# Kernel optimization log

Measured on AMD Instinct MI355X. Metric: run time of the kernel, lower is better.

## Reference

```python
import jax, jax.numpy as jnp
import numpy as np

NUM_HEADS = 12


def setup_inputs() -> dict:
    key = jax.random.key(0)
    ks = jax.random.split(key, 5)
    B, N, C = 64, 388, 768  # N = 8*8*2 + 16*16 + 4
    return {
        "x": jax.random.normal(ks[0], (B, N, C), dtype=jnp.float32),
        "qkv_w": jax.random.normal(ks[1], (3 * C, C), dtype=jnp.float32) * 0.02,
        "qkv_b": jax.random.normal(ks[2], (3 * C,), dtype=jnp.float32) * 0.02,
        "proj_w": jax.random.normal(ks[3], (C, C), dtype=jnp.float32) * 0.02,
        "proj_b": jax.random.normal(ks[4], (C,), dtype=jnp.float32) * 0.02,
        "t_h": 8, "t_w": 8, "s_h": 16, "s_w": 16,
    }


def reference(x, qkv_w, qkv_b, proj_w, proj_b, t_h, t_w, s_h, s_w):
    B, N, C = x.shape
    H = NUM_HEADS
    D = C // H
    scale = D ** -0.5
    L_t = t_h * t_w * 2          # template (x2) tokens
    L_s = s_h * s_w + 4          # search tokens + 4 extra

    qkv = x @ qkv_w.T + qkv_b                       # [B,N,3C]
    qkv = qkv.reshape(B, N, 3, H, D).transpose(2, 0, 3, 1, 4)  # [3,B,H,N,D]
    q, k, v = qkv[0], qkv[1], qkv[2]                # each [B,H,N,D]

    q_mt, q_s = q[:, :, :L_t], q[:, :, L_t:]
    k_mt = k[:, :, :L_t]
    v_mt = v[:, :, :L_t]

    # template self-attention (template queries attend only to template keys)
    attn_mt = jax.nn.softmax(jnp.einsum("bhqd,bhkd->bhqk", q_mt, k_mt) * scale, axis=-1)
    x_mt = jnp.einsum("bhqk,bhkd->bhqd", attn_mt, v_mt)  # [B,H,L_t,D]
    x_mt = x_mt.transpose(0, 2, 1, 3).reshape(B, L_t, C)

    # search queries attend to ALL keys
    attn_s = jax.nn.softmax(jnp.einsum("bhqd,bhkd->bhqk", q_s, k) * scale, axis=-1)
    x_s = jnp.einsum("bhqk,bhkd->bhqd", attn_s, v)  # [B,H,L_s,D]
    x_s = x_s.transpose(0, 2, 1, 3).reshape(B, L_s, C)

    out = jnp.concatenate([x_mt, x_s], axis=1)      # [B,N,C]
    out = out @ proj_w.T + proj_b
    return out
```

## Files before the change

kernel.cpp:

```cpp
#include <hip/hip_runtime.h>
#include <cstdint>
#include <cstddef>
#include <cmath>

typedef __attribute__((ext_vector_type(4))) float f32x4;
typedef __attribute__((ext_vector_type(8))) short bf16x8;

typedef const __attribute__((address_space(1))) void* gas_ptr;
typedef __attribute__((address_space(3))) void* las_ptr;

static __device__ __forceinline__ short f2bf(float f) {
    __bf16 h = (__bf16)f;
    return __builtin_bit_cast(short, h);
}

constexpr int MP = 25088;

__global__ void cvt_all(const float* __restrict__ x,  const float* __restrict__ qw,
                        const float* __restrict__ pw,
                        short* __restrict__ xb, short* __restrict__ qwb,
                        short* __restrict__ pwb)
{
    constexpr int NX = MP * 768 / 4;
    constexpr int NQ = 2304 * 768 / 4;
    constexpr int NP = 768 * 768 / 4;
    constexpr int NT = NX + NQ + NP;
    int i = blockIdx.x * blockDim.x + threadIdx.x;
    const int stride = gridDim.x * blockDim.x;
    for (; i < NT; i += stride) {
        if (i < NX) {
            const int flat = i * 4;
            const int mp  = flat / 768;
            const int col = flat - mp * 768;
            const int b   = mp / 392;
            const int nn  = mp - b * 392;
            short4 o;
            if (nn < 388) {
                const float4 v = *reinterpret_cast<const float4*>(
                    x + ((size_t)(b * 388 + nn) * 768 + col));
                o.x = f2bf(v.x); o.y = f2bf(v.y); o.z = f2bf(v.z); o.w = f2bf(v.w);
            } else {
                o.x = 0; o.y = 0; o.z = 0; o.w = 0;
            }
            reinterpret_cast<short4*>(xb)[i] = o;
        } else if (i < NX + NQ) {
            const int j = i - NX;
            const float4 v = reinterpret_cast<const float4*>(qw)[j];
            short4 o;
            o.x = f2bf(v.x); o.y = f2bf(v.y); o.z = f2bf(v.z); o.w = f2bf(v.w);
            reinterpret_cast<short4*>(qwb)[j] = o;
        } else {
            const int j = i - NX - NQ;
            const float4 v = reinterpret_cast<const float4*>(pw)[j];
            short4 o;
            o.x = f2bf(v.x); o.y = f2bf(v.y); o.z = f2bf(v.z); o.w = f2bf(v.w);
            reinterpret_cast<short4*>(pwb)[j] = o;
        }
    }
}

__global__ __launch_bounds__(512, 2) void gemm_qkv256(
    const short* __restrict__ A, const short* __restrict__ Bw,
    const float* __restrict__ bias,
    short* __restrict__ qk, short* __restrict__ vT)
{
    constexpr int K = 768;
    constexpr int KT = 12;
    __shared__ __align__(16) short lds[2][2][256 * 64];

    const int tid  = threadIdx.x;
    const int lane = tid & 63;
    const int wid  = tid >> 6;
    const int lrow = lane & 15;
    const int lgrp = lane >> 4;
    const int wr   = wid >> 2;
    const int wc   = wid & 3;

    const int nwg = gridDim.x;
    const int q8  = nwg >> 3, r8 = nwg & 7;
    const int xcd = blockIdx.x & 7, bidx = blockIdx.x >> 3;
    const int wgid = (xcd < r8 ? xcd * (q8 + 1) : r8 * (q8 + 1) + (xcd - r8) * q8) + bidx;
    constexpr int G = 14, SG = G * 9;
    const int mg  = wgid / SG;
    const int r_  = wgid - mg * SG;
    const int nn_ = r_ / G;
    const int mi  = r_ - nn_ * G;
    const int m0  = (mg * G + mi) * 256;
    const int n0  = nn_ * 256;

    f32x4 acc[8][4];
    #pragma unroll
    for (int i = 0; i < 8; ++i)
        #pragma unroll
        for (int j = 0; j < 4; ++j)
            acc[i][j] = f32x4{0.f, 0.f, 0.f, 0.f};

    auto stage = [&](int kt, int buf) {
        #pragma unroll
        for (int it = 0; it < 4; ++it) {
            const int c   = it * 512 + tid;
            const int row = c >> 3;
            const int scb = ((c & 7) * 16) ^ ((row & 7) << 4);
            const short* ga = A  + (size_t)(m0 + row) * K + kt * 64 + (scb >> 1);
            const short* gb = Bw + (size_t)(n0 + row) * K + kt * 64 + (scb >> 1);
            __builtin_amdgcn_global_load_lds((gas_ptr)ga, (las_ptr)((char*)&lds[buf][0][0] + c * 16), 16, 0, 0);
            __builtin_amdgcn_global_load_lds((gas_ptr)gb, (las_ptr)((char*)&lds[buf][1][0] + c * 16), 16, 0, 0);
        }
    };

    stage(0, 0);

    for (int kt = 0; kt < KT; ++kt) {
        const int cur = kt & 1;
        if (kt + 1 < KT) {
            stage(kt + 1, cur ^ 1);
            asm volatile("s_waitcnt vmcnt(8)" ::: "memory");
        } else {
            asm volatile("s_waitcnt vmcnt(0)" ::: "memory");
        }
        __builtin_amdgcn_s_barrier();
        __builtin_amdgcn_sched_barrier(0);

        #pragma unroll
        for (int ks = 0; ks < 2; ++ks) {
            bf16x8 af[8], bfv[4];
            #pragma unroll
            for (int i = 0; i < 8; ++i) {
                const int r   = wr * 128 + i * 16 + lrow;
                const int byt = r * 128 + ((ks * 64 + lgrp * 16) ^ ((r & 7) << 4));
                af[i] = *reinterpret_cast<const bf16x8*>((const char*)&lds[cur][0][0] + byt);
            }
            #pragma unroll
            for (int j = 0; j < 4; ++j) {
                const int r   = wc * 64 + j * 16 + lrow;
                const int byt = r * 128 + ((ks * 64 + lgrp * 16) ^ ((r & 7) << 4));
                bfv[j] = *reinterpret_cast<const bf16x8*>((const char*)&lds[cur][1][0] + byt);
            }
            #pragma unroll
            for (int i = 0; i < 8; ++i)
                #pragma unroll
                for (int j = 0; j < 4; ++j)
                    acc[i][j] = __builtin_amdgcn_mfma_f32_16x16x32_bf16(af[i], bfv[j], acc[i][j], 0, 0, 0);
        }

        __builtin_amdgcn_sched_barrier(0);
        __builtin_amdgcn_s_barrier();
    }

    const int mb = m0 + wr * 128;
    const int nb = n0 + wc * 64;
    if (n0 < 1536) {
        #pragma unroll
        for (int j = 0; j < 4; ++j) {
            const int c  = nb + j * 16 + lrow;
            const float sc = (c < 768) ? 0.18033688011116f : 1.0f;
            const float bv = bias[c];
            #pragma unroll
            for (int i = 0; i < 8; ++i) {
                #pragma unroll
                for (int r = 0; r < 4; ++r) {
                    const int m = mb + i * 16 + lgrp * 4 + r;
                    qk[(size_t)m * 1536 + c] = f2bf((acc[i][j][r] + bv) * sc);
                }
            }
        }
    } else {
        const int h = (nb - 1536) >> 6;
        short* lw = (short*)&lds[0][0][0] + wid * (64 * 80);
        #pragma unroll
        for (int pass = 0; pass < 2; ++pass) {
            if (pass) {
                asm volatile("s_waitcnt lgkmcnt(0)" ::: "memory");
                __builtin_amdgcn_sched_barrier(0);
            }
            #pragma unroll
            for (int j = 0; j < 4; ++j) {
                const int dloc = j * 16 + lrow;
                const float bv = bias[nb + j * 16 + lrow];
                #pragma unroll
                for (int ii = 0; ii < 4; ++ii)
                    #pragma unroll
                    for (int r = 0; r < 4; ++r)
                        lw[dloc * 80 + ii * 16 + lgrp * 4 + r] = f2bf(acc[pass * 4 + ii][j][r] + bv);
            }
            asm volatile("s_waitcnt lgkmcnt(0)" ::: "memory");
            __builtin_amdgcn_sched_barrier(0);
            #pragma unroll
            for (int w = 0; w < 8; ++w) {
                const int d    = w * 8 + (lane >> 3);
                const int nloc = (lane & 7) * 8;
                const bf16x8 val = *reinterpret_cast<const bf16x8*>(lw + d * 80 + nloc);
                const int mchunk = mb + pass * 64 + nloc;
                const int b  = mchunk / 392;
                const int nn = mchunk - b * 392;
                short* dst = vT + ((size_t)(b * 12 + h) * 64 + d) * 392 + nn;
                *reinterpret_cast<bf16x8*>(dst) = val;
            }
        }
    }
}

__global__ __launch_bounds__(256) void gemm_proj(
    const short* __restrict__ A, const short* __restrict__ Bw,
    const float* __restrict__ bias, float* __restrict__ fo, int NB)
{
    constexpr int K = 768;
    constexpr int KT = 12;
    __shared__ __align__(16) short ldsraw[2 * 128 * 64 * 2];
    short* ldsA = ldsraw;
    short* ldsB = ldsraw + 2 * 128 * 64;

    const int tid  = threadIdx.x;
    const int lane = tid & 63;
    const int wid  = tid >> 6;
    const int lrow = lane & 15;
    const int lgrp = lane >> 4;
    const int wr   = wid >> 1;
    const int wc   = wid & 1;

    const int nwg = gridDim.x;
    const int q8  = nwg >> 3, r8 = nwg & 7;
    const int xcd = blockIdx.x & 7, bidx = blockIdx.x >> 3;
    const int wgid = (xcd < r8 ? xcd * (q8 + 1) : r8 * (q8 + 1) + (xcd - r8) * q8) + bidx;
    const int m0 = (wgid / NB) * 128;
    const int n0 = (wgid % NB) * 128;

    f32x4 acc[4][4];
    #pragma unroll
    for (int i = 0; i < 4; ++i)
        #pragma unroll
        for (int j = 0; j < 4; ++j)
            acc[i][j] = f32x4{0.f, 0.f, 0.f, 0.f};

    auto stage = [&](int kt, int buf) {
        #pragma unroll
        for (int it = 0; it < 4; ++it) {
            const int c   = it * 256 + wid * 64 + lane;
            const int row = c >> 3;
            const int scb = ((c & 7) * 16) ^ ((row & 7) << 4);
            const short* ga = A  + (size_t)(m0 + row) * K + kt * 64 + (scb >> 1);
            const short* gb = Bw + (size_t)(n0 + row) * K + kt * 64 + (scb >> 1);
            __builtin_amdgcn_global_load_lds((gas_ptr)ga, (las_ptr)((char*)(ldsA + buf * 128 * 64) + c * 16), 16, 0, 0);
            __builtin_amdgcn_global_load_lds((gas_ptr)gb, (las_ptr)((char*)(ldsB + buf * 128 * 64) + c * 16), 16, 0, 0);
        }
    };

    stage(0, 0);

    for (int kt = 0; kt < KT; ++kt) {
        const int cur = kt & 1;
        if (kt + 1 < KT) {
            stage(kt + 1, cur ^ 1);
            asm volatile("s_waitcnt vmcnt(8)" ::: "memory");
        } else {
            asm volatile("s_waitcnt vmcnt(0)" ::: "memory");
        }
        __builtin_amdgcn_s_barrier();
        __builtin_amdgcn_sched_barrier(0);

        #pragma unroll
        for (int ks = 0; ks < 2; ++ks) {
            bf16x8 af[4], bfv[4];
            #pragma unroll
            for (int i = 0; i < 4; ++i) {
                const int r   = wr * 64 + i * 16 + lrow;
                const int byt = r * 128 + ((ks * 64 + lgrp * 16) ^ ((r & 7) << 4));
                af[i] = *reinterpret_cast<const bf16x8*>((const char*)(ldsA + cur * 128 * 64) + byt);
            }
            #pragma unroll
            for (int j = 0; j < 4; ++j) {
                const int r   = wc * 64 + j * 16 + lrow;
                const int byt = r * 128 + ((ks * 64 + lgrp * 16) ^ ((r & 7) << 4));
                bfv[j] = *reinterpret_cast<const bf16x8*>((const char*)(ldsB + cur * 128 * 64) + byt);
            }
            #pragma unroll
            for (int i = 0; i < 4; ++i)
                #pragma unroll
                for (int j = 0; j < 4; ++j)
                    acc[i][j] = __builtin_amdgcn_mfma_f32_16x16x32_bf16(af[i], bfv[j], acc[i][j], 0, 0, 0);
        }

        __builtin_amdgcn_sched_barrier(0);
        __builtin_amdgcn_s_barrier();
    }

    const int mb = m0 + wr * 64;
    const int nb = n0 + wc * 64;
    #pragma unroll
    for (int i = 0; i < 4; ++i) {
        #pragma unroll
        for (int r = 0; r < 4; ++r) {
            const int m = mb + i * 16 + lgrp * 4 + r;
            #pragma unroll
            for (int j = 0; j < 4; ++j) {
                const int c = nb + j * 16 + lrow;
                fo[(size_t)m * 768 + c] = acc[i][j][r] + bias[c];
            }
        }
    }
}

constexpr int PSTRB = 128;

static __device__ __forceinline__ void attn_chunk64(
    int kbeg, int k_len,
    const short* __restrict__ klds, const short* __restrict__ vlds,
    const bf16x8 (&qf)[2], char* __restrict__ my,
    int lrow, int lgrp,
    float& rs, f32x4 (&oacc)[4])
{
    f32x4 sacc[4];
    #pragma unroll
    for (int t = 0; t < 4; ++t) sacc[t] = f32x4{0.f, 0.f, 0.f, 0.f};

    #pragma unroll
    for (int t = 0; t < 4; ++t) {
        const int kl   = t * 16 + lrow;
        const int byt0 = kl * 128 + ((lgrp * 16) ^ ((kl & 7) << 4));
        const int byt1 = kl * 128 + ((64 + lgrp * 16) ^ ((kl & 7) << 4));
        const bf16x8 k0 = *reinterpret_cast<const bf16x8*>((const char*)klds + byt0);
        const bf16x8 k1 = *reinterpret_cast<const bf16x8*>((const char*)klds + byt1);
        sacc[t] = __builtin_amdgcn_mfma_f32_16x16x32_bf16(k0, qf[0], sacc[t], 0, 0, 0);
        sacc[t] = __builtin_amdgcn_mfma_f32_16x16x32_bf16(k1, qf[1], sacc[t], 0, 0, 0);
    }

    if (kbeg + 64 <= k_len) {
        #pragma unroll
        for (int t = 0; t < 4; ++t) {
            short4 pk;
            #pragma unroll
            for (int r = 0; r < 4; ++r) {
                const float p = exp2f(sacc[t][r]);
                rs += p;
                ((short*)&pk)[r] = f2bf(p);
            }
            const int byt = lrow * PSTRB + ((t * 32 + lgrp * 8) ^ ((lrow & 7) << 4));
            *reinterpret_cast<short4*>(my + byt) = pk;
        }
    } else {
        #pragma unroll
        for (int t = 0; t < 4; ++t) {
            short4 pk;
            #pragma unroll
            for (int r = 0; r < 4; ++r) {
                const int key = kbeg + t * 16 + lgrp * 4 + r;
                const float p = (key < k_len) ? exp2f(sacc[t][r]) : 0.f;
                rs += p;
                ((short*)&pk)[r] = f2bf(p);
            }
            const int byt = lrow * PSTRB + ((t * 32 + lgrp * 8) ^ ((lrow & 7) << 4));
            *reinterpret_cast<short4*>(my + byt) = pk;
        }
    }

    #pragma unroll
    for (int ks = 0; ks < 2; ++ks) {
        const bf16x8 pf = *reinterpret_cast<const bf16x8*>(
            my + lrow * PSTRB + ((ks * 64 + lgrp * 16) ^ ((lrow & 7) << 4)));
        #pragma unroll
        for (int dt = 0; dt < 4; ++dt) {
            const int d = dt * 16 + lrow;
            const bf16x8 vf = *reinterpret_cast<const bf16x8*>(
                (const char*)vlds + d * 128 + ((ks * 64 + lgrp * 16) ^ ((d & 7) << 4)));
            oacc[dt] = __builtin_amdgcn_mfma_f32_16x16x32_bf16(pf, vf, oacc[dt], 0, 0, 0);
        }
    }
}

__global__ __launch_bounds__(256, 4) void attn_flash(
    const short* __restrict__ qkb, const short* __restrict__ vT,
    short* __restrict__ ao)
{
    __shared__ __align__(16) short klds[2][64 * 64];
    __shared__ __align__(16) short vlds[2][64 * 64];
    __shared__ __align__(16) char  plds[4][16 * PSTRB];

    const int tid  = threadIdx.x;
    const int lane = tid & 63;
    const int wid  = tid >> 6;
    const int lrow = lane & 15;
    const int lgrp = lane >> 4;

    const int blk = blockIdx.x;
    const int xcd = blk & 7;
    const int i7  = blk >> 3;
    const int bh  = xcd * 96 + i7 / 7;
    const int bx  = i7 % 7;

    int q_start, qend, k_len, nch;
    if (bx < 2) { q_start = bx * 64;             qend = 128; k_len = 128; nch = 2; }
    else        { q_start = 128 + (bx - 2) * 64; qend = 388; k_len = 388; nch = 7; }

    const int q0 = q_start + wid * 16;

    const int b = bh / 12, h = bh - b * 12;
    const short* qbase = qkb + (size_t)b * 392 * 1536 + h * 64;
    const short* kbase = qbase + 768;
    const short* vbase = vT + (size_t)bh * 64 * 392;

    int qrow = q0 + lrow; if (qrow >= qend) qrow = qend - 1;
    bf16x8 qf[2];
    #pragma unroll
    for (int ks = 0; ks < 2; ++ks)
        qf[ks] = *reinterpret_cast<const bf16x8*>(qbase + (size_t)qrow * 1536 + ks * 32 + lgrp * 8);

    float rs = 0.f;
    f32x4 oacc[4];
    #pragma unroll
    for (int dt = 0; dt < 4; ++dt) oacc[dt] = f32x4{0.f, 0.f, 0.f, 0.f};

    char* my = &plds[wid][0];

    auto stage64 = [&](int ch, int buf) {
        const int kbeg = ch * 64;
        #pragma unroll
        for (int it = 0; it < 2; ++it) {
            const int c = it * 256 + tid;
            const int krow = c >> 3;
            const int scb = ((c & 7) * 16) ^ ((krow & 7) << 4);
            int g = kbeg + krow; if (g > 391) g = 391;
            const short* gk = kbase + (size_t)g * 1536 + (scb >> 1);
            __builtin_amdgcn_global_load_lds((gas_ptr)gk, (las_ptr)((char*)&klds[buf][0] + c * 16), 16, 0, 0);
        }
        #pragma unroll
        for (int it = 0; it < 2; ++it) {
            const int c = it * 256 + tid;
            const int vrow = c >> 3;
            const int scb = ((c & 7) * 16) ^ ((vrow & 7) << 4);
            const short* gv = vbase + (size_t)vrow * 392 + kbeg + (scb >> 1);
            __builtin_amdgcn_global_load_lds((gas_ptr)gv, (las_ptr)((char*)&vlds[buf][0] + c * 16), 16, 0, 0);
        }
    };

    stage64(0, 0);

    for (int ch = 0; ch < nch; ++ch) {
        const int cur = ch & 1;
        if (ch + 1 < nch) {
            stage64(ch + 1, cur ^ 1);
            asm volatile("s_waitcnt vmcnt(4)" ::: "memory");
        } else {
            asm volatile("s_waitcnt vmcnt(0)" ::: "memory");
        }
        __builtin_amdgcn_s_barrier();
        __builtin_amdgcn_sched_barrier(0);

        attn_chunk64(ch * 64, k_len, &klds[cur][0], &vlds[cur][0],
                     qf, my, lrow, lgrp, rs, oacc);

        __builtin_amdgcn_sched_barrier(0);
        __builtin_amdgcn_s_barrier();
    }

    rs += __shfl_xor(rs, 16, 64);
    rs += __shfl_xor(rs, 32, 64);

    float inv[4];
    #pragma unroll
    for (int r = 0; r < 4; ++r) inv[r] = 1.0f / __shfl(rs, lgrp * 4 + r, 64);

    #pragma unroll
    for (int r = 0; r < 4; ++r) {
        const int qn = q0 + lgrp * 4 + r;
        if (qn < qend) {
            #pragma unroll
            for (int dt = 0; dt < 4; ++dt)
                ao[((size_t)b * 388 + qn) * 768 + h * 64 + dt * 16 + lrow] =
                    f2bf(oacc[dt][r] * inv[r]);
        }
    }
}

extern "C" void kernel_launch(void* const* d_in, const int* in_sizes, int n_in,
                              void* d_out, int out_size, void* d_ws, size_t ws_size,
                              hipStream_t stream) {
    (void)in_sizes; (void)n_in; (void)out_size; (void)ws_size;
    const float* x      = (const float*)d_in[0];
    const float* qkv_w  = (const float*)d_in[1];
    const float* qkv_b  = (const float*)d_in[2];
    const float* proj_w = (const float*)d_in[3];
    const float* proj_b = (const float*)d_in[4];
    float* out = (float*)d_out;

    char* ws = (char*)d_ws;
    short* xb   = (short*)(ws);
    short* attn = (short*)(ws);
    short* qkb  = (short*)(ws + 38535168);
    short* vTb  = (short*)(ws + 115605504);
    short* qwb  = (short*)(ws + 154140672);
    short* pwb  = (short*)(ws + 157679616);

    cvt_all<<<2048, 256, 0, stream>>>(x, qkv_w, proj_w, xb, qwb, pwb);

    gemm_qkv256<<<dim3(98 * 9), 512, 0, stream>>>(xb, qwb, qkv_b, qkb, vTb);

    attn_flash<<<dim3(5376), 256, 0, stream>>>(qkb, vTb, attn);

    gemm_proj<<<dim3(194 * 6), 256, 0, stream>>>(attn, pwb, proj_b, out, 6);
}
```

Baseline: 229.9 us.

## Rewrite QKV GEMM with 128x128 tiles and A fragments loaded into registers

Replaces the 256x256-tile, 512-thread QKV GEMM with a 128x128-tile, 256-thread kernel. In the new kernel each wave loads its A rows directly from global memory into registers and only B is staged in LDS through a double-buffered, manually unrolled pipeline. The aim is to cut LDS traffic and footprint and raise occupancy to three blocks per CU. In exchange, A gets less reuse across waves, the grid is four times larger, and the V-transpose epilogue is rewritten for the new tile shape.

```diff
diff --git a/kernel.cpp b/kernel.cpp
--- a/kernel.cpp
+++ b/kernel.cpp
@@ -59,143 +59,158 @@
     }
 }
 
-__global__ __launch_bounds__(512, 2) void gemm_qkv256(
+__global__ __launch_bounds__(256, 3) void gemm_qkv_areg(
     const short* __restrict__ A, const short* __restrict__ Bw,
     const float* __restrict__ bias,
     short* __restrict__ qk, short* __restrict__ vT)
 {
     constexpr int K = 768;
-    constexpr int KT = 12;
-    __shared__ __align__(16) short lds[2][2][256 * 64];
+    __shared__ __align__(16) short ldsB[2][128 * 64];
 
     const int tid  = threadIdx.x;
     const int lane = tid & 63;
     const int wid  = tid >> 6;
     const int lrow = lane & 15;
     const int lgrp = lane >> 4;
-    const int wr   = wid >> 2;
-    const int wc   = wid & 3;
 
     const int nwg = gridDim.x;
     const int q8  = nwg >> 3, r8 = nwg & 7;
     const int xcd = blockIdx.x & 7, bidx = blockIdx.x >> 3;
     const int wgid = (xcd < r8 ? xcd * (q8 + 1) : r8 * (q8 + 1) + (xcd - r8) * q8) + bidx;
-    constexpr int G = 14, SG = G * 9;
-    const int mg  = wgid / SG;
-    const int r_  = wgid - mg * SG;
-    const int nn_ = r_ / G;
-    const int mi  = r_ - nn_ * G;
-    const int m0  = (mg * G + mi) * 256;
-    const int n0  = nn_ * 256;
-
-    f32x4 acc[8][4];
-    #pragma unroll
-    for (int i = 0; i < 8; ++i)
-        #pragma unroll
-        for (int j = 0; j < 4; ++j)
+
+    constexpr int G = 14, SG = G * 18;
+    const int mg = wgid / SG;
+    const int r_ = wgid - mg * SG;
+    const int n_ = r_ / G;
+    const int mi = r_ - n_ * G;
+    const int m0 = (mg * G + mi) * 128;
+    const int n0 = n_ * 128;
+
+    f32x4 acc[2][8];
+    #pragma unroll
+    for (int i = 0; i < 2; ++i)
+        #pragma unroll
+        for (int j = 0; j < 8; ++j)
             acc[i][j] = f32x4{0.f, 0.f, 0.f, 0.f};
 
-    auto stage = [&](int kt, int buf) {
+    const short* arow0 = A + (size_t)(m0 + wid * 32 + lrow) * K;
+    const short* arow1 = arow0 + (size_t)16 * K;
+
+    auto loadA = [&](int kt, bf16x8 (&dst)[2][2]) {
+        #pragma unroll
+        for (int ks = 0; ks < 2; ++ks) {
+            dst[0][ks] = *reinterpret_cast<const bf16x8*>(arow0 + kt * 64 + ks * 32 + lgrp * 8);
+            dst[1][ks] = *reinterpret_cast<const bf16x8*>(arow1 + kt * 64 + ks * 32 + lgrp * 8);
+        }
+    };
+    auto stageB = [&](int kt, int buf) {
         #pragma unroll
         for (int it = 0; it < 4; ++it) {
-            const int c   = it * 512 + tid;
+            const int c   = it * 256 + tid;
             const int row = c >> 3;
             const int scb = ((c & 7) * 16) ^ ((row & 7) << 4);
-            const short* ga = A  + (size_t)(m0 + row) * K + kt * 64 + (scb >> 1);
             const short* gb = Bw + (size_t)(n0 + row) * K + kt * 64 + (scb >> 1);
-            __builtin_amdgcn_global_load_lds((gas_ptr)ga, (las_ptr)((char*)&lds[buf][0][0] + c * 16), 16, 0, 0);
-            __builtin_amdgcn_global_load_lds((gas_ptr)gb, (las_ptr)((char*)&lds[buf][1][0] + c * 16), 16, 0, 0);
+            __builtin_amdgcn_global_load_lds((gas_ptr)gb, (las_ptr)((char*)&ldsB[buf][0] + c * 16), 16, 0, 0);
         }
     };
-
-    stage(0, 0);
-
-    for (int kt = 0; kt < KT; ++kt) {
-        const int cur = kt & 1;
-        if (kt + 1 < KT) {
-            stage(kt + 1, cur ^ 1);
-            asm volatile("s_waitcnt vmcnt(8)" ::: "memory");
-        } else {
-            asm volatile("s_waitcnt vmcnt(0)" ::: "memory");
-        }
-        __builtin_amdgcn_s_barrier();
-        __builtin_amdgcn_sched_barrier(0);
-
+    auto compute = [&](int buf, const bf16x8 (&af)[2][2]) {
         #pragma unroll
         for (int ks = 0; ks < 2; ++ks) {
-            bf16x8 af[8], bfv[4];
-            #pragma unroll
-            for (int i = 0; i < 8; ++i) {
-                const int r   = wr * 128 + i * 16 + lrow;
+            bf16x8 bfv[8];
+            #pragma unroll
+            for (int j = 0; j < 8; ++j) {
+                const int r   = j * 16 + lrow;
                 const int byt = r * 128 + ((ks * 64 + lgrp * 16) ^ ((r & 7) << 4));
-                af[i] = *reinterpret_cast<const bf16x8*>((const char*)&lds[cur][0][0] + byt);
-            }
-            #pragma unroll
-            for (int j = 0; j < 4; ++j) {
-                const int r   = wc * 64 + j * 16 + lrow;
-                const int byt = r * 128 + ((ks * 64 + lgrp * 16) ^ ((r & 7) << 4));
-                bfv[j] = *reinterpret_cast<const bf16x8*>((const char*)&lds[cur][1][0] + byt);
-            }
-            #pragma unroll
-            for (int i = 0; i < 8; ++i)
+                bfv[j] = *reinterpret_cast<const bf16x8*>((const char*)&ldsB[buf][0] + byt);
+            }
+            #pragma unroll
+            for (int i = 0; i < 2; ++i)
                 #pragma unroll
-                for (int j = 0; j < 4; ++j)
-                    acc[i][j] = __builtin_amdgcn_mfma_f32_16x16x32_bf16(af[i], bfv[j], acc[i][j], 0, 0, 0);
-        }
-
-        __builtin_amdgcn_sched_barrier(0);
-        __builtin_amdgcn_s_barrier();
-    }
-
-    const int mb = m0 + wr * 128;
-    const int nb = n0 + wc * 64;
+                for (int j = 0; j < 8; ++j)
+                    acc[i][j] = __builtin_amdgcn_mfma_f32_16x16x32_bf16(af[i][ks], bfv[j], acc[i][j], 0, 0, 0);
+        }
+    };
+
+    bf16x8 afX[2][2], afY[2][2];
+
+    loadA(0, afX);
+    stageB(0, 0);
+    asm volatile("s_waitcnt vmcnt(0)" ::: "memory");
+    __builtin_amdgcn_s_barrier();
+    __builtin_amdgcn_sched_barrier(0);
+
+    #pragma unroll 1
+    for (int u = 0; u < 6; ++u) {
+        loadA(2 * u + 1, afY);
+        stageB(2 * u + 1, 1);
+        __builtin_amdgcn_sched_barrier(0);
+        asm volatile("s_waitcnt vmcnt(8)" ::: "memory");
+        __builtin_amdgcn_s_barrier();
+        __builtin_amdgcn_sched_barrier(0);
+        compute(0, afX);
+        __builtin_amdgcn_sched_barrier(0);
+        __builtin_amdgcn_s_barrier();
+
+        const bool more = (2 * u + 2 < 12);
+        if (more) {
+            loadA(2 * u + 2, afX);
+            stageB(2 * u + 2, 0);
+        }
+        __builtin_amdgcn_sched_barrier(0);
+        if (more) asm volatile("s_waitcnt vmcnt(8)" ::: "memory");
+        else      asm volatile("s_waitcnt vmcnt(0)" ::: "memory");
+        __builtin_amdgcn_s_barrier();
+        __builtin_amdgcn_sched_barrier(0);
+        compute(1, afY);
+        __builtin_amdgcn_sched_barrier(0);
+        __builtin_amdgcn_s_barrier();
+    }
+
+    const int mrow = m0 + wid * 32;
     if (n0 < 1536) {
         #pragma unroll
-        for (int j = 0; j < 4; ++j) {
-            const int c  = nb + j * 16 + lrow;
+        for (int j = 0; j < 8; ++j) {
+            const int c  = n0 + j * 16 + lrow;
             const float sc = (c < 768) ? 0.18033688011116f : 1.0f;
             const float bv = bias[c];
             #pragma unroll
-            for (int i = 0; i < 8; ++i) {
+            for (int i = 0; i < 2; ++i) {
                 #pragma unroll
                 for (int r = 0; r < 4; ++r) {
-                    const int m = mb + i * 16 + lgrp * 4 + r;
+                    const int m = mrow + i * 16 + lgrp * 4 + r;
                     qk[(size_t)m * 1536 + c] = f2bf((acc[i][j][r] + bv) * sc);
                 }
             }
         }
     } else {
-        const int h = (nb - 1536) >> 6;
-        short* lw = (short*)&lds[0][0][0] + wid * (64 * 80);
-        #pragma unroll
-        for (int pass = 0; pass < 2; ++pass) {
-            if (pass) {
-                asm volatile("s_waitcnt lgkmcnt(0)" ::: "memory");
-                __builtin_amdgcn_sched_barrier(0);
-            }
-            #pragma unroll
-            for (int j = 0; j < 4; ++j) {
-                const int dloc = j * 16 + lrow;
-                const float bv = bias[nb + j * 16 + lrow];
+        const int hb = (n0 - 1536) >> 6;
+        short* lw = &ldsB[0][0] + wid * 4096;
+        #pragma unroll
+        for (int j = 0; j < 8; ++j) {
+            const int colLocal = j * 16 + lrow;
+            const float bv = bias[n0 + colLocal];
+            #pragma unroll
+            for (int i = 0; i < 2; ++i)
                 #pragma unroll
-                for (int ii = 0; ii < 4; ++ii)
-                    #pragma unroll
-                    for (int r = 0; r < 4; ++r)
-                        lw[dloc * 80 + ii * 16 + lgrp * 4 + r] = f2bf(acc[pass * 4 + ii][j][r] + bv);
-            }
-            asm volatile("s_waitcnt lgkmcnt(0)" ::: "memory");
-            __builtin_amdgcn_sched_barrier(0);
-            #pragma unroll
-            for (int w = 0; w < 8; ++w) {
-                const int d    = w * 8 + (lane >> 3);
-                const int nloc = (lane & 7) * 8;
-                const bf16x8 val = *reinterpret_cast<const bf16x8*>(lw + d * 80 + nloc);
-                const int mchunk = mb + pass * 64 + nloc;
-                const int b  = mchunk / 392;
-                const int nn = mchunk - b * 392;
-                short* dst = vT + ((size_t)(b * 12 + h) * 64 + d) * 392 + nn;
-                *reinterpret_cast<bf16x8*>(dst) = val;
-            }
+                for (int r = 0; r < 4; ++r) {
+                    const int n = i * 16 + lgrp * 4 + r;
+                    lw[colLocal * 32 + n] = f2bf(acc[i][j][r] + bv);
+                }
+        }
+        asm volatile("s_waitcnt lgkmcnt(0)" ::: "memory");
+        __builtin_amdgcn_sched_barrier(0);
+        #pragma unroll
+        for (int it = 0; it < 8; ++it) {
+            const int colLocal = it * 16 + (lane >> 2);
+            const int nloc     = (lane & 3) * 8;
+            const bf16x8 val = *reinterpret_cast<const bf16x8*>(lw + colLocal * 32 + nloc);
+            const int h = hb + (colLocal >> 6);
+            const int d = colLocal & 63;
+            const int mchunk = mrow + nloc;
+            const int b  = mchunk / 392;
+            const int nn = mchunk - b * 392;
+            short* dst = vT + ((size_t)(b * 12 + h) * 64 + d) * 392 + nn;
+            *reinterpret_cast<bf16x8*>(dst) = val;
         }
     }
 }
@@ -492,7 +507,7 @@
 
     cvt_all<<<2048, 256, 0, stream>>>(x, qkv_w, proj_w, xb, qwb, pwb);
 
-    gemm_qkv256<<<dim3(98 * 9), 512, 0, stream>>>(xb, qwb, qkv_b, qkb, vTb);
+    gemm_qkv_areg<<<dim3(196 * 18), 256, 0, stream>>>(xb, qwb, qkv_b, qkb, vTb);
 
     attn_flash<<<dim3(5376), 256, 0, stream>>>(qkb, vTb, attn);
 
```

Result: slower. 259.6 us (+12.9%).
